# Kernel tuning notes

Measured on AMD Instinct MI355X. Metric: run time of the kernel, lower is better.

The kernel has to match this reference:

```python
import jax, jax.numpy as jnp
import numpy as np

D_MODEL = 1024
NUM_HEADS = 16
D_K = D_MODEL // NUM_HEADS  # 64
THETA = 10000.0
BATCH = 2
SEQ = 2048


def _rope_tables(positions, d_k, theta):
    # freq_k = theta**(-2k/d_k), each repeated twice (interleaved layout)
    k = jnp.arange(d_k // 2, dtype=jnp.float32)
    freq = theta ** (-2.0 * k / d_k)            # [d_k/2]
    freq = jnp.repeat(freq, 2)                  # [d_k], pattern f0,f0,f1,f1,...
    ang = positions.astype(jnp.float32)[:, None] * freq[None, :]  # [s, d_k]
    return jnp.cos(ang), jnp.sin(ang)


def _apply_rope(x, cos, sin):
    # x: [b, h, s, d_k]; interleaved rotation: y[0::2]=-x[1::2], y[1::2]=x[0::2]
    x1 = x[..., 0::2]
    x2 = x[..., 1::2]
    y = jnp.stack([-x2, x1], axis=-1).reshape(x.shape)
    return x * cos + y * sin


def setup_inputs() -> dict:
    key = jax.random.key(0)
    kx, kq, kk, kv, ko = jax.random.split(key, 5)
    sw = (2.0 / (2 * D_MODEL)) ** 0.5
    return {
        "x": jax.random.normal(kx, (BATCH, SEQ, D_MODEL), dtype=jnp.float32),
        "WQ": jax.random.normal(kq, (D_MODEL, D_MODEL), dtype=jnp.float32) * sw,
        "WK": jax.random.normal(kk, (D_MODEL, D_MODEL), dtype=jnp.float32) * sw,
        "WV": jax.random.normal(kv, (D_MODEL, D_MODEL), dtype=jnp.float32) * sw,
        "WO": jax.random.normal(ko, (D_MODEL, D_MODEL), dtype=jnp.float32) * sw,
        "token_positions": jnp.arange(SEQ, dtype=jnp.int32),
    }


def reference(x, WQ, WK, WV, WO, token_positions):
    b, s, d_model = x.shape
    h, d_k = NUM_HEADS, D_K

    # fused QKV projection: W = cat([WQ,WK,WV], 0); QKV = x @ W.T
    W = jnp.concatenate([WQ, WK, WV], axis=0)          # [3*d_model, d_model]
    QKV = jnp.einsum('bsd,ed->bse', x, W)              # [b, s, 3*d_model]
    Q, K, V = jnp.split(QKV, 3, axis=-1)               # each [b, s, d_model]

    def to_heads(t):
        return t.reshape(b, s, h, d_k).transpose(0, 2, 1, 3)  # [b, h, s, d_k]

    Q, K, V = to_heads(Q), to_heads(K), to_heads(V)

    cos, sin = _rope_tables(token_positions, d_k, THETA)       # [s, d_k]
    Q = _apply_rope(Q, cos, sin)
    K = _apply_rope(K, cos, sin)

    scale = 1.0 / jnp.sqrt(jnp.float32(d_k))
    scores = jnp.einsum('bhqd,bhkd->bhqk', Q, K) * scale       # [b,h,s,s]
    causal = jnp.tril(jnp.ones((s, s), dtype=bool))
    scores = jnp.where(causal[None, None], scores, -jnp.inf)
    probs = jax.nn.softmax(scores, axis=-1)
    attn = jnp.einsum('bhqk,bhkd->bhqd', probs, V)             # [b,h,s,d_k]
    attn = attn.transpose(0, 2, 1, 3).reshape(b, s, h * d_k)   # [b,s,d_model]
    return jnp.einsum('bsd,ed->bse', attn, WO)                 # [b,s,d_model]
```

## Files before the change

### kernel.cpp

```cpp
#include <hip/hip_runtime.h>
#include <hip/hip_bf16.h>
#include <math.h>

#define BATCH 2
#define SEQ 2048
#define DMODEL 1024
#define NHEADS 16
#define DK 64
#define BH (BATCH*NHEADS)
#define GK 1024

#define SCALE2 0.18033688011112042f
#define SHIFT  16.0f

typedef __bf16 bf16_t;
typedef __bf16 bf16x8 __attribute__((ext_vector_type(8)));
typedef __bf16 bf16x4 __attribute__((ext_vector_type(4)));
typedef float  floatx4 __attribute__((ext_vector_type(4)));

__device__ __forceinline__ void load_lds16(const bf16_t* g, bf16_t* l) {
    __builtin_amdgcn_global_load_lds(
        (const __attribute__((address_space(1))) void*)g,
        (__attribute__((address_space(3))) void*)l,
        16, 0, 0);
}

__global__ __launch_bounds__(256) void rope_tables_kernel(
    const int* __restrict__ pos, float2* __restrict__ csT)
{
    int idx = blockIdx.x * 256 + threadIdx.x;
    int kk = idx & 31, s = idx >> 5;
    float freq = exp2f((float)kk * (-13.287712379549449f / 32.0f));
    float ang = (float)pos[s] * freq;
    float sn, cs;
    sincosf(ang, &sn, &cs);
    csT[idx] = make_float2(cs, sn);
}

__global__ __launch_bounds__(256) void convert_all_kernel(
    const float* __restrict__ x,
    const float* __restrict__ WQ, const float* __restrict__ WK,
    const float* __restrict__ WV, const float* __restrict__ WO,
    bf16_t* __restrict__ xb, bf16_t* __restrict__ Wb)
{
    const int blk = blockIdx.x;
    const float* src;
    bf16_t* dst;
    int base;
    if (blk < 2048) {
        src = x; dst = xb; base = blk * 2048;
    } else {
        int wi  = (blk - 2048) >> 9;
        base = ((blk - 2048) & 511) * 2048;
        src = (wi == 0) ? WQ : (wi == 1) ? WK : (wi == 2) ? WV : WO;
        dst = Wb + (size_t)wi * DMODEL * DMODEL;
    }
    int i = base + threadIdx.x * 8;
    float4 a = *(const float4*)(src + i);
    float4 b = *(const float4*)(src + i + 4);
    bf16x8 o;
    o[0] = (bf16_t)a.x; o[1] = (bf16_t)a.y; o[2] = (bf16_t)a.z; o[3] = (bf16_t)a.w;
    o[4] = (bf16_t)b.x; o[5] = (bf16_t)b.y; o[6] = (bf16_t)b.z; o[7] = (bf16_t)b.w;
    *(bf16x8*)(dst + i) = o;
}

__device__ __forceinline__ void gemm128_mainloop(
    const bf16_t* __restrict__ Arows, const bf16_t* __restrict__ Brows,
    bf16_t (*As)[32], bf16_t (*Bs)[32], int tid, floatx4 acc[4][4])
{
    const int lane = tid & 63;
    const int w = tid >> 6;
    const int wm = w >> 1, wn = w & 1;
    const int r = lane & 15, q = lane >> 4;

    const int row0 = tid >> 2,         kc0 = (tid & 3) << 3;
    const int row1 = (tid + 256) >> 2, kc1 = kc0;

    for (int kt = 0; kt < GK; kt += 32) {
        __syncthreads();
        load_lds16(Arows + (size_t)row0 * GK + kt + kc0, &As[row0][kc0]);
        load_lds16(Arows + (size_t)row1 * GK + kt + kc1, &As[row1][kc1]);
        load_lds16(Brows + (size_t)row0 * GK + kt + kc0, &Bs[row0][kc0]);
        load_lds16(Brows + (size_t)row1 * GK + kt + kc1, &Bs[row1][kc1]);
        __syncthreads();

        bf16x8 af[4], bfr[4];
        #pragma unroll
        for (int i = 0; i < 4; ++i)
            af[i] = *(const bf16x8*)&As[wm * 64 + i * 16 + r][q << 3];
        #pragma unroll
        for (int j = 0; j < 4; ++j)
            bfr[j] = *(const bf16x8*)&Bs[wn * 64 + j * 16 + r][q << 3];

        #pragma unroll
        for (int i = 0; i < 4; ++i)
            #pragma unroll
            for (int j = 0; j < 4; ++j)
                acc[i][j] = __builtin_amdgcn_mfma_f32_16x16x32_bf16(
                    af[i], bfr[j], acc[i][j], 0, 0, 0);
    }
}

__global__ __launch_bounds__(256) void qkv_gemm_kernel(
    const bf16_t* __restrict__ x, const bf16_t* __restrict__ Wb,
    const float2* __restrict__ csT,
    bf16_t* __restrict__ Qh, bf16_t* __restrict__ Kh, bf16_t* __restrict__ Vt)
{
    __shared__ __align__(16) char qsmem[128 * 136 * 2];
    bf16_t (*As)[32]  = (bf16_t(*)[32])qsmem;
    bf16_t (*Bs)[32]  = (bf16_t(*)[32])(qsmem + 8192);
    bf16_t (*Tt)[136] = (bf16_t(*)[136])qsmem;

    const int tid = threadIdx.x;
    const int m0 = blockIdx.y * 128;
    const int n0g = blockIdx.x * 128;
    const int which = n0g >> 10;
    const int nl0 = n0g & 1023;
    const bf16_t* Wsel = Wb + (size_t)which * DMODEL * DMODEL;

    floatx4 acc[4][4];
    #pragma unroll
    for (int i = 0; i < 4; ++i)
        #pragma unroll
        for (int j = 0; j < 4; ++j)
            acc[i][j] = (floatx4){0.f, 0.f, 0.f, 0.f};

    gemm128_mainloop(x + (size_t)m0 * GK, Wsel + (size_t)nl0 * GK, As, Bs, tid, acc);
    __syncthreads();

    const int w = tid >> 6, lane = tid & 63;
    const int wm = w >> 1, wn = w & 1;
    const int r = lane & 15, qd = lane >> 4;

    if (which < 2) {
        #pragma unroll
        for (int i = 0; i < 4; ++i)
            #pragma unroll
            for (int j = 0; j < 4; ++j)
                #pragma unroll
                for (int reg = 0; reg < 4; ++reg)
                    Tt[wm * 64 + i * 16 + qd * 4 + reg][wn * 64 + j * 16 + r] =
                        (bf16_t)acc[i][j][reg];
        __syncthreads();

        bf16_t* dst = (which == 0) ? Qh : Kh;
        const float qsc = (which == 0) ? SCALE2 : 1.0f;
        #pragma unroll
        for (int k2 = 0; k2 < 8; ++k2) {
            int id = tid + 256 * k2;
            int rowm = id >> 4;
            int ch = id & 15;
            int m = m0 + rowm, b = m >> 11, s = m & 2047;
            int n = nl0 + ch * 8, h = n >> 6, dk = n & 63;
            bf16x8 v = *(const bf16x8*)&Tt[rowm][ch * 8];
            const float4* csp = (const float4*)&csT[(s << 5) + (dk >> 1)];
            float4 c01 = csp[0], c23 = csp[1];
            bf16x8 o;
            float e, od;
            e = (float)v[0] * qsc; od = (float)v[1] * qsc;
            o[0] = (bf16_t)(e * c01.x - od * c01.y); o[1] = (bf16_t)(od * c01.x + e * c01.y);
            e = (float)v[2] * qsc; od = (float)v[3] * qsc;
            o[2] = (bf16_t)(e * c01.z - od * c01.w); o[3] = (bf16_t)(od * c01.z + e * c01.w);
            e = (float)v[4] * qsc; od = (float)v[5] * qsc;
            o[4] = (bf16_t)(e * c23.x - od * c23.y); o[5] = (bf16_t)(od * c23.x + e * c23.y);
            e = (float)v[6] * qsc; od = (float)v[7] * qsc;
            o[6] = (bf16_t)(e * c23.z - od * c23.w); o[7] = (bf16_t)(od * c23.z + e * c23.w);
            *(bf16x8*)(dst + (((size_t)(b << 4) + h) * SEQ + s) * DK + dk) = o;
        }
    } else {
        #pragma unroll
        for (int i = 0; i < 4; ++i)
            #pragma unroll
            for (int j = 0; j < 4; ++j) {
                int n_local = wn * 64 + j * 16 + r;
                int m_base  = wm * 64 + i * 16 + qd * 4;
                bf16x4 t;
                #pragma unroll
                for (int reg = 0; reg < 4; ++reg) t[reg] = (bf16_t)acc[i][j][reg];
                *(bf16x4*)&Tt[n_local][m_base] = t;
            }
        __syncthreads();
        const int b = m0 >> 11, s0 = m0 & 2047;
        #pragma unroll
        for (int k2 = 0; k2 < 8; ++k2) {
            int id = tid + 256 * k2;
            int row = id >> 4;
            int ch  = id & 15;
            int n = nl0 + row, h = n >> 6, dk = n & 63;
            bf16x8 val = *(const bf16x8*)&Tt[row][ch * 8];
            *(bf16x8*)(Vt + (((size_t)(b << 4) + h) * DK + dk) * SEQ + s0 + ch * 8) = val;
        }
    }
}

__global__ __launch_bounds__(512, 4) void attn_mfma_kernel(
    const bf16_t* __restrict__ Qh, const bf16_t* __restrict__ Kh,
    const bf16_t* __restrict__ Vtg, bf16_t* __restrict__ attnO)
{
    __shared__ __align__(16) char smem[49152];
    bf16x8 (*Ks)[64][8]   = (bf16x8(*)[64][8])smem;
    bf16x8 (*Vs)[64][8]   = (bf16x8(*)[64][8])(smem + 16384);
    bf16x4 (*ps4)[16][16] = (bf16x4(*)[16][16])(smem + 32768);
    float  (*Om)[64][68]  = (float(*)[64][68])smem;
    float  (*lsum)[64]    = (float(*)[64])(smem + 34816);

    const int tid = threadIdx.x, w = tid >> 6, lane = tid & 63;
    const int grp = w >> 2, wv = w & 3;
    const int r = lane & 15, qd = lane >> 4;
    const int bh = blockIdx.y;
    const int t = tid & 255;
    const int row0 = t >> 3, c80 = (t & 7) * 8;

    const int R  = r & 7;
    const int R2 = R << 1;
    const int csw = (t & 7) ^ (row0 & 7);

    const bf16_t* Kbh = Kh  + (size_t)bh * SEQ * DK;
    const bf16_t* Vbh = Vtg + (size_t)bh * DK * SEQ;
    const int b = bh >> 4, h = bh & 15;

    bf16x8 ones;
    #pragma unroll
    for (int i = 0; i < 8; ++i) ones[i] = (bf16_t)1.0f;

    for (int half = 0; half < 2; ++half) {
        const int qt = half ? (int)blockIdx.x : (31 - (int)blockIdx.x);
        const int q0 = qt * 64;
        const int nIter = (qt >> 1) + 1;

        const bf16_t* Qbase = Qh + (((size_t)bh * SEQ) + q0 + wv * 16 + r) * DK;
        bf16x8 aq0 = *(const bf16x8*)(Qbase + qd * 8);
        bf16x8 aq1 = *(const bf16x8*)(Qbase + 32 + qd * 8);

        const int j0 = grp * 64;
        bf16x8 pk0 = *(const bf16x8*)(Kbh + (size_t)(j0 + row0) * DK + c80);
        bf16x8 pk1 = *(const bf16x8*)(Kbh + (size_t)(j0 + row0 + 32) * DK + c80);
        bf16x8 pv0 = *(const bf16x8*)(Vbh + (size_t)row0 * SEQ + j0 + c80);
        bf16x8 pv1 = *(const bf16x8*)(Vbh + (size_t)(row0 + 32) * SEQ + j0 + c80);

        floatx4 Oa[4];
        #pragma unroll
        for (int nd = 0; nd < 4; ++nd) Oa[nd] = (floatx4){0.f, 0.f, 0.f, 0.f};
        floatx4 acc_l = (floatx4){0.f, 0.f, 0.f, 0.f};

        for (int it = 0; it < nIter; ++it) {
            const int kb = 2 * it + grp;
            const bool active = (kb <= qt);
            __syncthreads();
            if (active) {
                Ks[grp][row0][csw]      = pk0;
                Ks[grp][row0 + 32][csw] = pk1;
                Vs[grp][row0][csw]      = pv0;
                Vs[grp][row0 + 32][csw] = pv1;
            }
            if (kb + 2 <= qt) {
                const int j0n = (kb + 2) * 64;
                pk0 = *(const bf16x8*)(Kbh + (size_t)(j0n + row0) * DK + c80);
                pk1 = *(const bf16x8*)(Kbh + (size_t)(j0n + row0 + 32) * DK + c80);
                pv0 = *(const bf16x8*)(Vbh + (size_t)row0 * SEQ + j0n + c80);
                pv1 = *(const bf16x8*)(Vbh + (size_t)(row0 + 32) * SEQ + j0n + c80);
            }
            __syncthreads();
            if (!active) continue;

            __builtin_amdgcn_s_setprio(1);
            floatx4 acc[4];
            #pragma unroll
            for (int nt = 0; nt < 4; ++nt) {
                bf16x8 bk0 = Ks[grp][nt * 16 + r][qd ^ R];
                bf16x8 bk1 = Ks[grp][nt * 16 + r][(4 + qd) ^ R];
                floatx4 a = (floatx4){-SHIFT, -SHIFT, -SHIFT, -SHIFT};
                a = __builtin_amdgcn_mfma_f32_16x16x32_bf16(bk0, aq0, a, 0, 0, 0);
                a = __builtin_amdgcn_mfma_f32_16x16x32_bf16(bk1, aq1, a, 0, 0, 0);
                acc[nt] = a;
            }

            if (kb == qt) {
                #pragma unroll
                for (int nt = 0; nt < 4; ++nt)
                    #pragma unroll
                    for (int rg = 0; rg < 4; ++rg)
                        if (nt * 16 + qd * 4 + rg > wv * 16 + r) acc[nt][rg] = -200.0f;
            }

            #pragma unroll
            for (int nt = 0; nt < 4; ++nt) {
                bf16x4 pkq;
                #pragma unroll
                for (int rg = 0; rg < 4; ++rg)
                    pkq[rg] = (bf16_t)exp2f(acc[nt][rg]);
                ps4[w][r][(nt * 4 + qd) ^ R2] = pkq;
            }
            asm volatile("" ::: "memory");
            __builtin_amdgcn_sched_barrier(0x7F);

            const int c0 = (qd * 2) ^ R2;
            const int c1 = (8 + qd * 2) ^ R2;
            bf16x4 p00 = ps4[w][r][c0], p01 = ps4[w][r][c0 + 1];
            bf16x4 p10 = ps4[w][r][c1], p11 = ps4[w][r][c1 + 1];
            bf16x8 ap0 = __builtin_shufflevector(p00, p01, 0, 1, 2, 3, 4, 5, 6, 7);
            bf16x8 ap1 = __builtin_shufflevector(p10, p11, 0, 1, 2, 3, 4, 5, 6, 7);

            acc_l = __builtin_amdgcn_mfma_f32_16x16x32_bf16(ap0, ones, acc_l, 0, 0, 0);
            acc_l = __builtin_amdgcn_mfma_f32_16x16x32_bf16(ap1, ones, acc_l, 0, 0, 0);

            #pragma unroll
            for (int nd = 0; nd < 4; ++nd) {
                bf16x8 bv0 = Vs[grp][nd * 16 + r][qd ^ R];
                bf16x8 bv1 = Vs[grp][nd * 16 + r][(4 + qd) ^ R];
                floatx4 c = Oa[nd];
                c = __builtin_amdgcn_mfma_f32_16x16x32_bf16(ap0, bv0, c, 0, 0, 0);
                c = __builtin_amdgcn_mfma_f32_16x16x32_bf16(ap1, bv1, c, 0, 0, 0);
                Oa[nd] = c;
            }
            __builtin_amdgcn_s_setprio(0);
        }

        __syncthreads();
        #pragma unroll
        for (int rg = 0; rg < 4; ++rg) {
            int rowq = wv * 16 + qd * 4 + rg;
            if (r == 0) lsum[grp][rowq] = acc_l[rg];
            #pragma unroll
            for (int nd = 0; nd < 4; ++nd)
                Om[grp][rowq][nd * 16 + r] = Oa[nd][rg];
        }
        __syncthreads();
        {
            int rowq = tid >> 3, c8 = (tid & 7) * 8;
            float inv = 1.0f / (lsum[0][rowq] + lsum[1][rowq]);
            float4 a0 = *(const float4*)&Om[0][rowq][c8];
            float4 a1 = *(const float4*)&Om[0][rowq][c8 + 4];
            float4 b0 = *(const float4*)&Om[1][rowq][c8];
            float4 b1 = *(const float4*)&Om[1][rowq][c8 + 4];
            bf16x8 o;
            o[0] = (bf16_t)((a0.x + b0.x) * inv);
            o[1] = (bf16_t)((a0.y + b0.y) * inv);
            o[2] = (bf16_t)((a0.z + b0.z) * inv);
            o[3] = (bf16_t)((a0.w + b0.w) * inv);
            o[4] = (bf16_t)((a1.x + b1.x) * inv);
            o[5] = (bf16_t)((a1.y + b1.y) * inv);
            o[6] = (bf16_t)((a1.z + b1.z) * inv);
            o[7] = (bf16_t)((a1.w + b1.w) * inv);
            int s = q0 + rowq;
            *(bf16x8*)(attnO + ((size_t)b * SEQ + s) * DMODEL + (h << 6) + c8) = o;
        }
    }
}

__global__ __launch_bounds__(256) void out_gemm_kernel(
    const bf16_t* __restrict__ attnI, const bf16_t* __restrict__ WOb,
    float* __restrict__ out)
{
    __shared__ __align__(16) bf16_t As[64][32];
    __shared__ __align__(16) bf16_t Bs[128][32];

    const int tid = threadIdx.x;
    const int m0 = blockIdx.y * 64;
    const int n0 = blockIdx.x * 128;
    const int lane = tid & 63, w = tid >> 6;
    const int wm = w >> 1, wn = w & 1;
    const int r = lane & 15, q = lane >> 4;

    const bf16_t* Arows = attnI + (size_t)m0 * GK;
    const bf16_t* Brows = WOb + (size_t)n0 * GK;
    const int rowA = tid >> 2, kc = (tid & 3) << 3;
    const int rowB1 = (tid + 256) >> 2;

    floatx4 acc[2][4];
    #pragma unroll
    for (int i = 0; i < 2; ++i)
        #pragma unroll
        for (int j = 0; j < 4; ++j)
            acc[i][j] = (floatx4){0.f, 0.f, 0.f, 0.f};

    for (int kt = 0; kt < GK; kt += 32) {
        __syncthreads();
        load_lds16(Arows + (size_t)rowA * GK + kt + kc, &As[rowA][kc]);
        load_lds16(Brows + (size_t)rowA * GK + kt + kc, &Bs[rowA][kc]);
        load_lds16(Brows + (size_t)rowB1 * GK + kt + kc, &Bs[rowB1][kc]);
        __syncthreads();

        bf16x8 af[2], bfr[4];
        #pragma unroll
        for (int i = 0; i < 2; ++i)
            af[i] = *(const bf16x8*)&As[wm * 32 + i * 16 + r][q << 3];
        #pragma unroll
        for (int j = 0; j < 4; ++j)
            bfr[j] = *(const bf16x8*)&Bs[wn * 64 + j * 16 + r][q << 3];

        #pragma unroll
        for (int i = 0; i < 2; ++i)
            #pragma unroll
            for (int j = 0; j < 4; ++j)
                acc[i][j] = __builtin_amdgcn_mfma_f32_16x16x32_bf16(
                    af[i], bfr[j], acc[i][j], 0, 0, 0);
    }

    #pragma unroll
    for (int i = 0; i < 2; ++i)
        #pragma unroll
        for (int j = 0; j < 4; ++j)
            #pragma unroll
            for (int reg = 0; reg < 4; ++reg) {
                int m = m0 + wm * 32 + i * 16 + q * 4 + reg;
                int n = n0 + wn * 64 + j * 16 + r;
                out[(size_t)m * DMODEL + n] = acc[i][j][reg];
            }
}

extern "C" void kernel_launch(void* const* d_in, const int* in_sizes, int n_in,
                              void* d_out, int out_size, void* d_ws, size_t ws_size,
                              hipStream_t stream)
{
    (void)in_sizes; (void)n_in; (void)out_size; (void)ws_size;

    const float* x  = (const float*)d_in[0];
    const float* WQ = (const float*)d_in[1];
    const float* WK = (const float*)d_in[2];
    const float* WV = (const float*)d_in[3];
    const float* WO = (const float*)d_in[4];
    const int* tpos = (const int*)d_in[5];
    float* out = (float*)d_out;

    bf16_t* xb   = (bf16_t*)d_ws;
    bf16_t* Wb   = xb + (size_t)BATCH * SEQ * DMODEL;
    bf16_t* Qh   = Wb + (size_t)4 * DMODEL * DMODEL;
    bf16_t* Kh   = Qh + (size_t)BH * SEQ * DK;
    bf16_t* Vt   = Kh + (size_t)BH * SEQ * DK;
    bf16_t* attn = Vt + (size_t)BH * SEQ * DK;
    float2* csT  = (float2*)(attn + (size_t)BATCH * SEQ * DMODEL);

    rope_tables_kernel<<<dim3(SEQ * 32 / 256), dim3(256), 0, stream>>>(tpos, csT);

    convert_all_kernel<<<dim3(4096), dim3(256), 0, stream>>>(
        x, WQ, WK, WV, WO, xb, Wb);

    qkv_gemm_kernel<<<dim3(3 * DMODEL / 128, BATCH * SEQ / 128), dim3(256), 0, stream>>>(
        xb, Wb, csT, Qh, Kh, Vt);

    attn_mfma_kernel<<<dim3(16, 32), dim3(512), 0, stream>>>(Qh, Kh, Vt, attn);

    out_gemm_kernel<<<dim3(DMODEL / 128, BATCH * SEQ / 64), dim3(256), 0, stream>>>(
        attn, Wb + (size_t)3 * DMODEL * DMODEL, out);
}
```

Measured before the change: 180.6 us.

## Permute K rows in LDS to keep P in registers; fuse rope-table kernel

K rows are stored in LDS in a permuted order, so each lane's QK^T MFMA output already sits in the A-operand layout the PV MFMA needs. The exponentiated probabilities are packed straight into registers, which drops the LDS write/read round trip for P and shrinks shared memory (possibly raising occupancy). The causal mask index is remapped to match the permutation. Separately, the rope-table computation is folded into the convert kernel as extra blocks, removing one kernel launch.

```diff
diff --git a/kernel.cpp b/kernel.cpp
--- a/kernel.cpp
+++ b/kernel.cpp
@@ -25,25 +25,24 @@
         16, 0, 0);
 }
 
-__global__ __launch_bounds__(256) void rope_tables_kernel(
-    const int* __restrict__ pos, float2* __restrict__ csT)
-{
-    int idx = blockIdx.x * 256 + threadIdx.x;
-    int kk = idx & 31, s = idx >> 5;
-    float freq = exp2f((float)kk * (-13.287712379549449f / 32.0f));
-    float ang = (float)pos[s] * freq;
-    float sn, cs;
-    sincosf(ang, &sn, &cs);
-    csT[idx] = make_float2(cs, sn);
-}
-
 __global__ __launch_bounds__(256) void convert_all_kernel(
     const float* __restrict__ x,
     const float* __restrict__ WQ, const float* __restrict__ WK,
     const float* __restrict__ WV, const float* __restrict__ WO,
-    bf16_t* __restrict__ xb, bf16_t* __restrict__ Wb)
+    bf16_t* __restrict__ xb, bf16_t* __restrict__ Wb,
+    const int* __restrict__ pos, float2* __restrict__ csT)
 {
     const int blk = blockIdx.x;
+    if (blk >= 4096) {
+        int idx = (blk - 4096) * 256 + threadIdx.x;
+        int kk = idx & 31, s = idx >> 5;
+        float freq = exp2f((float)kk * (-13.287712379549449f / 32.0f));
+        float ang = (float)pos[s] * freq;
+        float sn, cs;
+        sincosf(ang, &sn, &cs);
+        csT[idx] = make_float2(cs, sn);
+        return;
+    }
     const float* src;
     bf16_t* dst;
     int base;
@@ -197,10 +196,9 @@
     const bf16_t* __restrict__ Qh, const bf16_t* __restrict__ Kh,
     const bf16_t* __restrict__ Vtg, bf16_t* __restrict__ attnO)
 {
-    __shared__ __align__(16) char smem[49152];
+    __shared__ __align__(16) char smem[35328];
     bf16x8 (*Ks)[64][8]   = (bf16x8(*)[64][8])smem;
     bf16x8 (*Vs)[64][8]   = (bf16x8(*)[64][8])(smem + 16384);
-    bf16x4 (*ps4)[16][16] = (bf16x4(*)[16][16])(smem + 32768);
     float  (*Om)[64][68]  = (float(*)[64][68])smem;
     float  (*lsum)[64]    = (float(*)[64])(smem + 34816);
 
@@ -211,9 +209,10 @@
     const int t = tid & 255;
     const int row0 = t >> 3, c80 = (t & 7) * 8;
 
-    const int R  = r & 7;
-    const int R2 = R << 1;
-    const int csw = (t & 7) ^ (row0 & 7);
+    const int rk  = (((row0 >> 2) & 1) << 4) + (((row0 >> 3) & 3) << 2) + (row0 & 3);
+    const int R   = r & 7;
+    const int cswK = (t & 7) ^ (rk & 7);
+    const int cswV = (t & 7) ^ (row0 & 7);
 
     const bf16_t* Kbh = Kh  + (size_t)bh * SEQ * DK;
     const bf16_t* Vbh = Vtg + (size_t)bh * DK * SEQ;
@@ -248,10 +247,10 @@
             const bool active = (kb <= qt);
             __syncthreads();
             if (active) {
-                Ks[grp][row0][csw]      = pk0;
-                Ks[grp][row0 + 32][csw] = pk1;
-                Vs[grp][row0][csw]      = pv0;
-                Vs[grp][row0 + 32][csw] = pv1;
+                Ks[grp][rk][cswK]        = pk0;
+                Ks[grp][rk + 32][cswK]   = pk1;
+                Vs[grp][row0][cswV]      = pv0;
+                Vs[grp][row0 + 32][cswV] = pv1;
             }
             if (kb + 2 <= qt) {
                 const int j0n = (kb + 2) * 64;
@@ -279,27 +278,20 @@
                 #pragma unroll
                 for (int nt = 0; nt < 4; ++nt)
                     #pragma unroll
-                    for (int rg = 0; rg < 4; ++rg)
-                        if (nt * 16 + qd * 4 + rg > wv * 16 + r) acc[nt][rg] = -200.0f;
-            }
-
-            #pragma unroll
-            for (int nt = 0; nt < 4; ++nt) {
-                bf16x4 pkq;
-                #pragma unroll
-                for (int rg = 0; rg < 4; ++rg)
-                    pkq[rg] = (bf16_t)exp2f(acc[nt][rg]);
-                ps4[w][r][(nt * 4 + qd) ^ R2] = pkq;
-            }
-            asm volatile("" ::: "memory");
-            __builtin_amdgcn_sched_barrier(0x7F);
-
-            const int c0 = (qd * 2) ^ R2;
-            const int c1 = (8 + qd * 2) ^ R2;
-            bf16x4 p00 = ps4[w][r][c0], p01 = ps4[w][r][c0 + 1];
-            bf16x4 p10 = ps4[w][r][c1], p11 = ps4[w][r][c1 + 1];
-            bf16x8 ap0 = __builtin_shufflevector(p00, p01, 0, 1, 2, 3, 4, 5, 6, 7);
-            bf16x8 ap1 = __builtin_shufflevector(p10, p11, 0, 1, 2, 3, 4, 5, 6, 7);
+                    for (int rg = 0; rg < 4; ++rg) {
+                        int keyl = ((nt >> 1) << 5) + qd * 8 + ((nt & 1) << 2) + rg;
+                        if (keyl > wv * 16 + r) acc[nt][rg] = -200.0f;
+                    }
+            }
+
+            bf16x8 ap0, ap1;
+            #pragma unroll
+            for (int rg = 0; rg < 4; ++rg) {
+                ap0[rg]     = (bf16_t)exp2f(acc[0][rg]);
+                ap0[4 + rg] = (bf16_t)exp2f(acc[1][rg]);
+                ap1[rg]     = (bf16_t)exp2f(acc[2][rg]);
+                ap1[4 + rg] = (bf16_t)exp2f(acc[3][rg]);
+            }
 
             acc_l = __builtin_amdgcn_mfma_f32_16x16x32_bf16(ap0, ones, acc_l, 0, 0, 0);
             acc_l = __builtin_amdgcn_mfma_f32_16x16x32_bf16(ap1, ones, acc_l, 0, 0, 0);
@@ -431,10 +423,8 @@
     bf16_t* attn = Vt + (size_t)BH * SEQ * DK;
     float2* csT  = (float2*)(attn + (size_t)BATCH * SEQ * DMODEL);
 
-    rope_tables_kernel<<<dim3(SEQ * 32 / 256), dim3(256), 0, stream>>>(tpos, csT);
-
-    convert_all_kernel<<<dim3(4096), dim3(256), 0, stream>>>(
-        x, WQ, WK, WV, WO, xb, Wb);
+    convert_all_kernel<<<dim3(4096 + 256), dim3(256), 0, stream>>>(
+        x, WQ, WK, WV, WO, xb, Wb, tpos, csT);
 
     qkv_gemm_kernel<<<dim3(3 * DMODEL / 128, BATCH * SEQ / 128), dim3(256), 0, stream>>>(
         xb, Wb, csT, Qh, Kh, Vt);
```

After: 172.8 us. 1.05x faster.
